# Kernel tuning notes

Measured on AMD Instinct MI355X. Metric: run time of the kernel, lower is better.

Reference implementation:

```python
import jax, jax.numpy as jnp
import numpy as np

N_FFT = 512
HOP = N_FFT // 4  # torch.stft default hop_length
TWO_PI = 2.0 * np.pi


def _stft_phase(x):
    """torch.stft(x, n_fft=512, return_complex=True) phase: center reflect-pad,
    rectangular window, onesided rfft. Returns [F, T'] with F = n_fft//2+1."""
    pad = N_FFT // 2
    xp = jnp.pad(x, (pad, pad), mode='reflect')
    n_frames = (xp.shape[0] - N_FFT) // HOP + 1
    idx = (np.arange(n_frames, dtype=np.int32)[:, None] * HOP
           + np.arange(N_FFT, dtype=np.int32)[None, :])
    frames = xp[idx]                      # [T', n_fft]
    spec = jnp.fft.rfft(frames, axis=-1)  # [T', F]
    return jnp.angle(spec).T              # [F, T']


def _anti_wrap(x):
    return jnp.abs(x - jnp.round(x / TWO_PI) * TWO_PI)


def _gd(p):
    # banded matmul with gd_matrix == out[f] = p[f-1] - p[f], out[0] = -p[0]
    return jnp.concatenate([-p[:1], p[:-1] - p[1:]], axis=0)


def _iaf(p):
    # banded matmul with iaf_matrix along time axis
    return jnp.concatenate([-p[:, :1], p[:, :-1] - p[:, 1:]], axis=1)


def setup_inputs() -> dict:
    key = jax.random.key(0)
    k1, k2 = jax.random.split(key)
    T = 4194304  # 2^22 samples (~262 s @ 16 kHz)
    yd = jax.random.normal(k1, (T,), dtype=jnp.float32)
    td = jax.random.normal(k2, (T,), dtype=jnp.float32)
    return {"yd": yd, "td": td}


def reference(yd, td):
    pr = _stft_phase(yd)  # [F, T']
    pg = _stft_phase(td)
    ip_loss = jnp.mean(_anti_wrap(pr - pg))
    gd_loss = jnp.mean(_anti_wrap(_gd(pr) - _gd(pg)))
    iaf_loss = jnp.mean(_anti_wrap(_iaf(pr) - _iaf(pg)))
    return (ip_loss, gd_loss, iaf_loss)
```

## Files before the change

### kernel.cpp

```cpp
#include <hip/hip_runtime.h>
#include <math.h>

#define HOP     128
#define NSLOTS  256
#define FPW     8
#define PI_F    3.14159265358979323846f
#define PI2_F   1.57079632679489661923f
#define K8      0.70710678118654752440f

#define LDS_FENCE() do { __asm__ volatile("" ::: "memory"); \
                         __builtin_amdgcn_wave_barrier(); } while (0)

struct cpx { float x, y; };
__device__ __forceinline__ cpx cadd(cpx a, cpx b){ return {a.x+b.x, a.y+b.y}; }
__device__ __forceinline__ cpx csub(cpx a, cpx b){ return {a.x-b.x, a.y-b.y}; }
__device__ __forceinline__ cpx cmul(cpx a, cpx b){
    return {fmaf(a.x,b.x,-a.y*b.y), fmaf(a.x,b.y, a.y*b.x)};
}
__device__ __forceinline__ cpx cmulc(cpx a, cpx b){
    return {fmaf(a.x,b.x, a.y*b.y), fmaf(a.y,b.x,-a.x*b.y)};
}

__device__ __forceinline__ float abs_angle(float re, float im) {
    float a = fabsf(im), b = fabsf(re);
    float mn = fminf(a, b), mx = fmaxf(a, b);
    float t = __fdividef(mn, fmaxf(mx, 1e-37f));
    float t2 = t * t;
    float p = fmaf(t2, -0.0117212f, 0.05265332f);
    p = fmaf(t2, p, -0.11643287f);
    p = fmaf(t2, p, 0.19354346f);
    p = fmaf(t2, p, -0.33262347f);
    p = fmaf(t2, p, 0.99997726f);
    float r = t * p;
    r = (a > b) ? (PI2_F - r) : r;
    r = (re < 0.f) ? (PI_F - r) : r;
    return r;
}

__device__ __forceinline__ void dft8(cpx v[8]) {
    cpx a0=cadd(v[0],v[4]), a1=cadd(v[1],v[5]), a2=cadd(v[2],v[6]), a3=cadd(v[3],v[7]);
    cpx b0=csub(v[0],v[4]), b1=csub(v[1],v[5]), b2=csub(v[2],v[6]), b3=csub(v[3],v[7]);
    b1 = cpx{K8*(b1.x+b1.y), K8*(b1.y-b1.x)};
    b2 = cpx{b2.y, -b2.x};
    b3 = cpx{K8*(b3.y-b3.x), -K8*(b3.x+b3.y)};
    cpx c0=cadd(a0,a2), c2=csub(a0,a2);
    cpx c1=cadd(a1,a3), c3=csub(a1,a3); c3 = cpx{c3.y, -c3.x};
    cpx d0=cadd(b0,b2), d2=csub(b0,b2);
    cpx d1=cadd(b1,b3), d3=csub(b1,b3); d3 = cpx{d3.y, -d3.x};
    v[0]=cadd(c0,c1); v[4]=csub(c0,c1);
    v[2]=cadd(c2,c3); v[6]=csub(c2,c3);
    v[1]=cadd(d0,d1); v[5]=csub(d0,d1);
    v[3]=cadd(d2,d3); v[7]=csub(d2,d3);
}

__global__ __launch_bounds__(256, 4) void phase_loss_kernel(
        const float* __restrict__ y, const float* __restrict__ g,
        float* __restrict__ acc, int* __restrict__ ticket,
        float* __restrict__ out, int T, int n_frames, float inv_count) {
    __shared__ float2 xch_all[4][576];
    __shared__ float2 cl_all[4][258];
    __shared__ float wsum[3][4];
    __shared__ int is_last;

    const int tid  = threadIdx.x;
    const int lane = tid & 63;
    const int wid  = tid >> 6;
    float2* xch = xch_all[wid];
    float2* Cl  = cl_all[wid] + 1;

    cpx tw1[8], tw2[8];
    #pragma unroll
    for (int k = 0; k < 8; ++k) {
        float a1 = -(2.0f * PI_F / 512.0f) * (float)(lane * k);
        __sincosf(a1, &tw1[k].y, &tw1[k].x);
        float a2 = -(2.0f * PI_F / 64.0f) * (float)((lane & 7) * k);
        __sincosf(a2, &tw2[k].y, &tw2[k].x);
    }

    float ip = 0.f, gd = 0.f, iaf = 0.f;
    cpx Cp[5];
    const int tmax_int = (T - 256) / HOP;

    auto do_frame = [&](int t, bool accum, bool hp) {
        cpx v[8];
        const int base = t * HOP - 256 + lane;
        if (t >= 2 && t <= tmax_int) {
            #pragma unroll
            for (int r = 0; r < 8; ++r) {
                int j = base + r * 64;
                v[r].x = y[j]; v[r].y = g[j];
            }
        } else {
            #pragma unroll
            for (int r = 0; r < 8; ++r) {
                int j = base + r * 64;
                j = (j < 0) ? -j : j;
                j = (j >= T) ? (2 * T - 2 - j) : j;
                v[r].x = y[j]; v[r].y = g[j];
            }
        }
        dft8(v);
        #pragma unroll
        for (int k = 1; k < 8; ++k) v[k] = cmul(v[k], tw1[k]);
        LDS_FENCE();
        #pragma unroll
        for (int k = 0; k < 8; ++k)
            xch[k * 72 + lane] = make_float2(v[k].x, v[k].y);
        LDS_FENCE();
        {
            const int ra = (lane >> 3) * 72 + (lane & 7);
            #pragma unroll
            for (int r = 0; r < 8; ++r) {
                float2 tmp = xch[ra + r * 8];
                v[r] = cpx{tmp.x, tmp.y};
            }
        }
        dft8(v);
        #pragma unroll
        for (int k = 1; k < 8; ++k) v[k] = cmul(v[k], tw2[k]);
        LDS_FENCE();
        #pragma unroll
        for (int k = 0; k < 8; ++k)
            xch[k * 65 + lane] = make_float2(v[k].x, v[k].y);
        LDS_FENCE();
        {
            const int ra = (lane >> 3) * 65 + (lane & 7) * 8;
            #pragma unroll
            for (int r = 0; r < 8; ++r) {
                float2 tmp = xch[ra + r];
                v[r] = cpx{tmp.x, tmp.y};
            }
        }
        dft8(v);
        float2* Z = xch;
        LDS_FENCE();
        #pragma unroll
        for (int j = 0; j < 8; ++j)
            Z[lane + (j << 6)] = make_float2(v[j].x, v[j].y);
        LDS_FENCE();
        cpx Cc[5];
        #pragma unroll
        for (int jj = 0; jj < 5; ++jj) {
            const int f = lane + (jj << 6);
            float2 tmp = Z[(512 - f) & 511];
            float ur = v[jj].x + tmp.x, ui = v[jj].y - tmp.y;
            float vx = v[jj].x - tmp.x, vy = v[jj].y + tmp.y;
            Cc[jj].x = fmaf(ur, vy, -ui * vx);
            Cc[jj].y = fmaf(ur, vx,  ui * vy);
        }
        if (accum) {
            LDS_FENCE();
            #pragma unroll
            for (int jj = 0; jj < 4; ++jj)
                Cl[lane + (jj << 6)] = make_float2(Cc[jj].x, Cc[jj].y);
            if (lane == 0) Cl[256] = make_float2(Cc[4].x, Cc[4].y);
            LDS_FENCE();
            cpx cm[4];
            #pragma unroll
            for (int jj = 0; jj < 4; ++jj) {
                float2 tmp = Cl[lane + (jj << 6) - 1];
                cm[jj] = cpx{tmp.x, tmp.y};
            }
            float2 c255 = Cl[255];
            #pragma unroll
            for (int jj = 0; jj < 4; ++jj) {
                cpx cc = Cc[jj];
                float aw = abs_angle(cc.x, cc.y);
                ip += aw;
                cpx qg = cmulc(cm[jj], cc);
                float gt = abs_angle(qg.x, qg.y);
                gd += (jj == 0 && lane == 0) ? aw : gt;
                if (hp) {
                    cpx qi = cmulc(Cp[jj], cc);
                    iaf += abs_angle(qi.x, qi.y);
                } else {
                    iaf += aw;
                }
            }
            if (lane == 0) {
                cpx cc = Cc[4];
                float aw = abs_angle(cc.x, cc.y);
                ip += aw;
                cpx qg = cmulc(cpx{c255.x, c255.y}, cc);
                gd += abs_angle(qg.x, qg.y);
                if (hp) {
                    cpx qi = cmulc(Cp[4], cc);
                    iaf += abs_angle(qi.x, qi.y);
                } else {
                    iaf += aw;
                }
            }
        }
        #pragma unroll
        for (int jj = 0; jj < 5; ++jj) Cp[jj] = Cc[jj];
    };

    const int chain   = (blockIdx.x << 2) | wid;
    const int nchains = (int)(gridDim.x << 2);
    const int t0 = chain * FPW;
    int tend = t0 + FPW;
    if (chain == nchains - 1) tend = n_frames;
    const bool havep = (t0 > 0);

    if (havep) do_frame(t0 - 1, false, false);
    #pragma unroll 2
    for (int t = t0; t < tend; ++t)
        do_frame(t, true, havep || (t > t0));

    __syncthreads();
    for (int off = 32; off; off >>= 1) {
        ip  += __shfl_down(ip, off);
        gd  += __shfl_down(gd, off);
        iaf += __shfl_down(iaf, off);
    }
    if (lane == 0) { wsum[0][wid] = ip; wsum[1][wid] = gd; wsum[2][wid] = iaf; }
    __syncthreads();
    if (tid == 0) {
        const int slot = (int)(blockIdx.x & (NSLOTS - 1));
        atomicAdd(acc + 0 * NSLOTS + slot, wsum[0][0] + wsum[0][1] + wsum[0][2] + wsum[0][3]);
        atomicAdd(acc + 1 * NSLOTS + slot, wsum[1][0] + wsum[1][1] + wsum[1][2] + wsum[1][3]);
        atomicAdd(acc + 2 * NSLOTS + slot, wsum[2][0] + wsum[2][1] + wsum[2][2] + wsum[2][3]);
        __threadfence();
        is_last = (atomicAdd(ticket, 1) == (int)gridDim.x - 1);
    }
    __syncthreads();
    if (is_last) {
        for (int l = 0; l < 3; l++) {
            float vv = __hip_atomic_load(acc + l * NSLOTS + tid,
                                         __ATOMIC_RELAXED, __HIP_MEMORY_SCOPE_AGENT);
            for (int off = 32; off; off >>= 1) vv += __shfl_down(vv, off);
            if (lane == 0) wsum[l][wid] = vv;
        }
        __syncthreads();
        if (tid < 3)
            out[tid] = (wsum[tid][0] + wsum[tid][1] + wsum[tid][2] + wsum[tid][3]) * inv_count;
    }
}

extern "C" void kernel_launch(void* const* d_in, const int* in_sizes, int n_in,
                              void* d_out, int out_size, void* d_ws, size_t ws_size,
                              hipStream_t stream) {
    const float* y = (const float*)d_in[0];
    const float* g = (const float*)d_in[1];
    float* out = (float*)d_out;
    float* acc = (float*)d_ws;
    int* ticket = (int*)((char*)d_ws + 3 * NSLOTS * sizeof(float));
    const int T = in_sizes[0];
    const int n_frames = T / HOP + 1;
    int n_blocks = n_frames / (FPW * 4);
    if (n_blocks < 1) n_blocks = 1;

    hipMemsetAsync(d_ws, 0, 3 * NSLOTS * sizeof(float) + sizeof(int), stream);
    const float inv_count = 1.0f / (257.0f * (float)n_frames);
    phase_loss_kernel<<<n_blocks, 256, 0, stream>>>(y, g, acc, ticket, out,
                                                    T, n_frames, inv_count);
}
```

Baseline: 136.1 us.

## Recompute neighbor bins from Z, drop Cl LDS buffer, raise occupancy

Removes the per-wave Cl shared buffer and its two fences. The neighbor frequency bin needed for the group-delay term is now rebuilt from the FFT output already held in Z using the Hermitian split. Twiddle arrays shrink to seven entries, launch bounds ask for 8 blocks per CU, and frames per wave drop from 8 to 4, giving more parallel chains. The cost is extra LDS reads and arithmetic per bin, a tighter register budget that may spill, and more redundant warm-up frames per chain.

New measurement: 352.9 us. 159% more time.

```diff
diff --git a/kernel.cpp b/kernel.cpp
--- a/kernel.cpp
+++ b/kernel.cpp
@@ -3,7 +3,7 @@
 
 #define HOP     128
 #define NSLOTS  256
-#define FPW     8
+#define FPW     4
 #define PI_F    3.14159265358979323846f
 #define PI2_F   1.57079632679489661923f
 #define K8      0.70710678118654752440f
@@ -53,12 +53,11 @@
     v[3]=cadd(d2,d3); v[7]=csub(d2,d3);
 }
 
-__global__ __launch_bounds__(256, 4) void phase_loss_kernel(
+__global__ __launch_bounds__(256, 8) void phase_loss_kernel(
         const float* __restrict__ y, const float* __restrict__ g,
         float* __restrict__ acc, int* __restrict__ ticket,
         float* __restrict__ out, int T, int n_frames, float inv_count) {
     __shared__ float2 xch_all[4][576];
-    __shared__ float2 cl_all[4][258];
     __shared__ float wsum[3][4];
     __shared__ int is_last;
 
@@ -66,20 +65,26 @@
     const int lane = tid & 63;
     const int wid  = tid >> 6;
     float2* xch = xch_all[wid];
-    float2* Cl  = cl_all[wid] + 1;
-
-    cpx tw1[8], tw2[8];
+
+    cpx tw1[7], tw2[7];
     #pragma unroll
-    for (int k = 0; k < 8; ++k) {
+    for (int k = 1; k < 8; ++k) {
         float a1 = -(2.0f * PI_F / 512.0f) * (float)(lane * k);
-        __sincosf(a1, &tw1[k].y, &tw1[k].x);
+        __sincosf(a1, &tw1[k-1].y, &tw1[k-1].x);
         float a2 = -(2.0f * PI_F / 64.0f) * (float)((lane & 7) * k);
-        __sincosf(a2, &tw2[k].y, &tw2[k].x);
+        __sincosf(a2, &tw2[k-1].y, &tw2[k-1].x);
     }
 
     float ip = 0.f, gd = 0.f, iaf = 0.f;
     cpx Cp[5];
     const int tmax_int = (T - 256) / HOP;
+
+    auto herm_to_C = [&](float2 zk, float2 zn) -> cpx {
+        float ur = zk.x + zn.x, ui = zk.y - zn.y;
+        float vx = zk.x - zn.x, vy = zk.y + zn.y;
+        return cpx{fmaf(ur, vy, -ui * vx),
+                   fmaf(ur, vx,  ui * vy)};
+    };
 
     auto do_frame = [&](int t, bool accum, bool hp) {
         cpx v[8];
@@ -101,7 +106,7 @@
         }
         dft8(v);
         #pragma unroll
-        for (int k = 1; k < 8; ++k) v[k] = cmul(v[k], tw1[k]);
+        for (int k = 1; k < 8; ++k) v[k] = cmul(v[k], tw1[k-1]);
         LDS_FENCE();
         #pragma unroll
         for (int k = 0; k < 8; ++k)
@@ -117,7 +122,7 @@
         }
         dft8(v);
         #pragma unroll
-        for (int k = 1; k < 8; ++k) v[k] = cmul(v[k], tw2[k]);
+        for (int k = 1; k < 8; ++k) v[k] = cmul(v[k], tw2[k-1]);
         LDS_FENCE();
         #pragma unroll
         for (int k = 0; k < 8; ++k)
@@ -142,32 +147,18 @@
         #pragma unroll
         for (int jj = 0; jj < 5; ++jj) {
             const int f = lane + (jj << 6);
-            float2 tmp = Z[(512 - f) & 511];
-            float ur = v[jj].x + tmp.x, ui = v[jj].y - tmp.y;
-            float vx = v[jj].x - tmp.x, vy = v[jj].y + tmp.y;
-            Cc[jj].x = fmaf(ur, vy, -ui * vx);
-            Cc[jj].y = fmaf(ur, vx,  ui * vy);
+            Cc[jj] = herm_to_C(make_float2(v[jj].x, v[jj].y),
+                               Z[(512 - f) & 511]);
         }
         if (accum) {
-            LDS_FENCE();
-            #pragma unroll
-            for (int jj = 0; jj < 4; ++jj)
-                Cl[lane + (jj << 6)] = make_float2(Cc[jj].x, Cc[jj].y);
-            if (lane == 0) Cl[256] = make_float2(Cc[4].x, Cc[4].y);
-            LDS_FENCE();
-            cpx cm[4];
             #pragma unroll
             for (int jj = 0; jj < 4; ++jj) {
-                float2 tmp = Cl[lane + (jj << 6) - 1];
-                cm[jj] = cpx{tmp.x, tmp.y};
-            }
-            float2 c255 = Cl[255];
-            #pragma unroll
-            for (int jj = 0; jj < 4; ++jj) {
+                const int f = lane + (jj << 6);
                 cpx cc = Cc[jj];
                 float aw = abs_angle(cc.x, cc.y);
                 ip += aw;
-                cpx qg = cmulc(cm[jj], cc);
+                cpx cm = herm_to_C(Z[(f - 1) & 511], Z[(513 - f) & 511]);
+                cpx qg = cmulc(cm, cc);
                 float gt = abs_angle(qg.x, qg.y);
                 gd += (jj == 0 && lane == 0) ? aw : gt;
                 if (hp) {
@@ -181,7 +172,8 @@
                 cpx cc = Cc[4];
                 float aw = abs_angle(cc.x, cc.y);
                 ip += aw;
-                cpx qg = cmulc(cpx{c255.x, c255.y}, cc);
+                cpx cm = herm_to_C(Z[255], Z[257]);
+                cpx qg = cmulc(cm, cc);
                 gd += abs_angle(qg.x, qg.y);
                 if (hp) {
                     cpx qi = cmulc(Cp[4], cc);
```
